# Optimization experiments

Measured on AMD Instinct MI355X. Metric: run time of the kernel, lower is better.

Reference implementation:

```python
import jax, jax.numpy as jnp
import numpy as np

B, S, D, H = 2, 2048, 1024, 16
HD = D // H

def setup_inputs() -> dict:
    key = jax.random.key(0)
    ks = jax.random.split(key, 5)
    s = 1.0 / np.sqrt(D)
    return {
        "x": jax.random.normal(ks[0], (B, S, D), dtype=jnp.float32),
        "Wq": jax.random.normal(ks[1], (D, D), dtype=jnp.float32) * s,
        "Wk": jax.random.normal(ks[2], (D, D), dtype=jnp.float32) * s,
        "Wv": jax.random.normal(ks[3], (D, D), dtype=jnp.float32) * s,
        "Wo": jax.random.normal(ks[4], (D, D), dtype=jnp.float32) * s,
        "bo": jnp.zeros((D,), dtype=jnp.float32),
    }

def reference(x, Wq, Wk, Wv, Wo, bo):
    b, n, _ = x.shape
    # QKV projections (no bias), reshape to [B, H, S, HD]
    def proj(W):
        return (x @ W.T).reshape(b, n, H, HD).transpose(0, 2, 1, 3)
    q, k, v = proj(Wq), proj(Wk), proj(Wv)
    scores = jnp.einsum("bhqd,bhkd->bhqk", q, k)
    causal = jnp.triu(jnp.ones((n, n), dtype=bool), k=1)
    scores = jnp.where(causal, -jnp.inf, scores)
    attn = jax.nn.softmax(scores / np.sqrt(HD), axis=-1)  # dropout p=0.0 (eval)
    ctx = jnp.einsum("bhqk,bhkd->bhqd", attn, v)
    ctx = ctx.transpose(0, 2, 1, 3).reshape(b, n, D)
    return ctx @ Wo.T + bo
```

## Files before the change

### kernel.cpp

```cpp
#include <hip/hip_runtime.h>
#include <stdint.h>


typedef __bf16 bf16_t;
typedef __bf16 bf16x8 __attribute__((ext_vector_type(8)));
typedef float  f32x4  __attribute__((ext_vector_type(4)));
typedef uint32_t u32x4 __attribute__((ext_vector_type(4)));

#define MFMA16(A, B, C) __builtin_amdgcn_mfma_f32_16x16x32_bf16(A, B, C, 0, 0, 0)

__device__ __forceinline__ void async_ld16(const bf16_t* g, bf16_t* l) {
  __builtin_amdgcn_global_load_lds(
      (const __attribute__((address_space(1))) void*)g,
      (__attribute__((address_space(3))) void*)l, 16, 0, 0);
}

__global__ __launch_bounds__(256) void cvt_x(const float* __restrict__ s,
                                             bf16_t* __restrict__ d) {
  const int i4 = (blockIdx.x * 256 + threadIdx.x) * 4;
  const float4 v = *(const float4*)(s + i4);
  union { uint64_t u; bf16_t h[4]; } pk;
  pk.h[0] = (bf16_t)v.x; pk.h[1] = (bf16_t)v.y;
  pk.h[2] = (bf16_t)v.z; pk.h[3] = (bf16_t)v.w;
  *(uint64_t*)(d + i4) = pk.u;
}

__global__ __launch_bounds__(256) void cvt_w3(
    const float* __restrict__ s0, const float* __restrict__ s1,
    const float* __restrict__ s2, bf16_t* __restrict__ d0,
    bf16_t* __restrict__ d1, bf16_t* __restrict__ d2) {
  const int z = blockIdx.y;
  const float* s = (z == 0) ? s0 : (z == 1) ? s1 : s2;
  bf16_t*      d = (z == 0) ? d0 : (z == 1) ? d1 : d2;
  const int i4 = (blockIdx.x * 256 + threadIdx.x) * 4;
  const float4 v = *(const float4*)(s + i4);
  union { uint64_t u; bf16_t h[4]; } pk;
  pk.h[0] = (bf16_t)v.x; pk.h[1] = (bf16_t)v.y;
  pk.h[2] = (bf16_t)v.z; pk.h[3] = (bf16_t)v.w;
  *(uint64_t*)(d + i4) = pk.u;
}

__device__ __forceinline__ void gemm_core_async(const bf16_t* __restrict__ A,
                                                const bf16_t* __restrict__ W,
                                                bf16_t* __restrict__ D,
                                                float* __restrict__ Dout,
                                                const float* __restrict__ bias,
                                                int mode) {
  __shared__ __align__(16) bf16_t As[128 * 64];
  __shared__ __align__(16) bf16_t Bs[128 * 64];

  const int tid  = threadIdx.x;
  const int lane = tid & 63;
  const int w    = tid >> 6;
  const int quad = lane >> 4;
  const int l15  = lane & 15;
  const int bm   = blockIdx.y * 128;
  const int bn   = blockIdx.x * 128;
  const int wm   = (w >> 1) * 64;
  const int wn   = (w & 1) * 64;
  const int sr   = lane >> 3;
  const int sc   = lane & 7;

  f32x4 acc[4][4] = {};

  for (int k0 = 0; k0 < 1024; k0 += 64) {
#pragma unroll
    for (int j = 0; j < 4; ++j) {
      const int r0 = w * 32 + j * 8;
      const int r  = r0 + sr;
      const int c  = sc ^ (r & 7);
      async_ld16(A + (size_t)(bm + r) * 1024 + k0 + c * 8, &As[r0 * 64]);
      async_ld16(W + (size_t)(bn + r) * 1024 + k0 + c * 8, &Bs[r0 * 64]);
    }
    __syncthreads();
#pragma unroll
    for (int kk = 0; kk < 64; kk += 32) {
      const int ck = (kk >> 3) + quad;
      bf16x8 aF[4], bF[4];
#pragma unroll
      for (int mt = 0; mt < 4; ++mt) {
        const int r = wm + mt * 16 + l15;
        aF[mt] = *(const bf16x8*)&As[r * 64 + (ck ^ (r & 7)) * 8];
      }
#pragma unroll
      for (int nt = 0; nt < 4; ++nt) {
        const int r = wn + nt * 16 + l15;
        bF[nt] = *(const bf16x8*)&Bs[r * 64 + (ck ^ (r & 7)) * 8];
      }
#pragma unroll
      for (int mt = 0; mt < 4; ++mt)
#pragma unroll
        for (int nt = 0; nt < 4; ++nt)
          acc[mt][nt] = MFMA16(aF[mt], bF[nt], acc[mt][nt]);
    }
    __syncthreads();
  }

#pragma unroll
  for (int mt = 0; mt < 4; ++mt) {
#pragma unroll
    for (int nt = 0; nt < 4; ++nt) {
      const int n  = bn + wn + nt * 16 + l15;
      const int mb = bm + wm + mt * 16 + quad * 4;
      if (mode == 0) {
        const int h = n >> 6, hd = n & 63;
#pragma unroll
        for (int r = 0; r < 4; ++r) {
          const int m = mb + r;
          const int b = m >> 11, s = m & 2047;
          D[(size_t)b * 2097152 + (size_t)h * 131072 + (size_t)s * 64 + hd] =
              (bf16_t)acc[mt][nt][r];
        }
      } else if (mode == 1) {
        const int h = n >> 6, hd = n & 63;
        const int b = mb >> 11, s0 = mb & 2047;
        union { uint64_t u; bf16_t h4[4]; } pk;
#pragma unroll
        for (int r = 0; r < 4; ++r) pk.h4[r] = (bf16_t)acc[mt][nt][r];
        *(uint64_t*)(D + (size_t)b * 2097152 + (size_t)h * 131072 +
                     (size_t)hd * 2048 + s0) = pk.u;
      } else {
        const float bv = bias[n];
#pragma unroll
        for (int r = 0; r < 4; ++r) {
          const int m = mb + r;
          Dout[(size_t)m * 1024 + n] = acc[mt][nt][r] + bv;
        }
      }
    }
  }
}

__global__ __launch_bounds__(256, 2) void gemm_qkv_a(
    const bf16_t* __restrict__ X,  const bf16_t* __restrict__ Wq,
    const bf16_t* __restrict__ Wk, const bf16_t* __restrict__ Wv,
    bf16_t* __restrict__ Q, bf16_t* __restrict__ K, bf16_t* __restrict__ V) {
  const int z = blockIdx.z;
  const bf16_t* W = (z == 0) ? Wq : (z == 1) ? Wk : Wv;
  bf16_t*       D = (z == 0) ? Q  : (z == 1) ? K  : V;
  gemm_core_async(X, W, D, nullptr, nullptr, (z == 2) ? 1 : 0);
}

__global__ __launch_bounds__(256, 2) void gemm_out_a(
    const bf16_t* __restrict__ ctx, const bf16_t* __restrict__ Wo,
    float* __restrict__ out, const float* __restrict__ bo) {
  gemm_core_async(ctx, Wo, nullptr, out, bo, 2);
}

__global__ __launch_bounds__(256, 2) void attn(
    const bf16_t* __restrict__ Qw, const bf16_t* __restrict__ Kw,
    const bf16_t* __restrict__ Vw, bf16_t* __restrict__ ctx) {
  constexpr int LDK = 72, LDV = 136, LDP = 136;
  __shared__ __align__(16) bf16_t Ks[128 * LDK];
  __shared__ __align__(16) bf16_t Vts[64 * LDV];
  __shared__ __align__(16) bf16_t Ps[128 * LDP];

  const int tid  = threadIdx.x;
  const int lane = tid & 63;
  const int w    = tid >> 6;
  const int quad = lane >> 4;
  const int l15  = lane & 15;
  const int b    = blockIdx.z;
  const int qt   = (b == 0) ? blockIdx.x : 15 - blockIdx.x;
  const int h    = blockIdx.y;
  const size_t bh = (size_t)(b * 16 + h) * (size_t)(2048 * 64);
  const bf16_t* Qh = Qw + bh;
  const bf16_t* Kh = Kw + bh;
  const bf16_t* Vh = Vw + bh;

  const int srow = tid >> 3, schk = tid & 7;
  const int vrow = tid >> 4, vchk = tid & 15;

  bf16_t* Qs = Ps;
  {
    u32x4 rq[4];
#pragma unroll
    for (int s2 = 0; s2 < 4; ++s2)
      rq[s2] = *(const u32x4*)(Qh + (size_t)(qt * 128 + srow + s2 * 32) * 64 + schk * 8);
#pragma unroll
    for (int s2 = 0; s2 < 4; ++s2)
      *(u32x4*)&Qs[(srow + s2 * 32) * LDK + schk * 8] = rq[s2];
  }
  __syncthreads();
  bf16x8 qF[2][2];
#pragma unroll
  for (int kq = 0; kq < 2; ++kq)
#pragma unroll
    for (int k2 = 0; k2 < 2; ++k2)
      qF[kq][k2] = *(const bf16x8*)
          &Qs[(w * 32 + kq * 16 + l15) * LDK + k2 * 32 + quad * 8];

  f32x4 O[2][4] = {};
  float mrow[2] = {-1e30f, -1e30f};
  float lrow[2] = {0.f, 0.f};

  const float sc_log2 = 0.125f * 1.44269504088896340736f;

  u32x4 rk[4], rv[4];
#pragma unroll
  for (int s2 = 0; s2 < 4; ++s2)
    rk[s2] = *(const u32x4*)(Kh + (size_t)(srow + s2 * 32) * 64 + schk * 8);
#pragma unroll
  for (int s2 = 0; s2 < 4; ++s2)
    rv[s2] = *(const u32x4*)(Vh + (size_t)(vrow + s2 * 16) * 2048 + vchk * 8);

  for (int kt = 0; kt <= qt; ++kt) {
    __syncthreads();
#pragma unroll
    for (int s2 = 0; s2 < 4; ++s2)
      *(u32x4*)&Ks[(srow + s2 * 32) * LDK + schk * 8] = rk[s2];
#pragma unroll
    for (int s2 = 0; s2 < 4; ++s2)
      *(u32x4*)&Vts[(vrow + s2 * 16) * LDV + vchk * 8] = rv[s2];
    __syncthreads();

    if (kt < qt) {
      const int kn = kt + 1;
#pragma unroll
      for (int s2 = 0; s2 < 4; ++s2)
        rk[s2] = *(const u32x4*)(Kh + (size_t)(kn * 128 + srow + s2 * 32) * 64 + schk * 8);
#pragma unroll
      for (int s2 = 0; s2 < 4; ++s2)
        rv[s2] = *(const u32x4*)(Vh + (size_t)(vrow + s2 * 16) * 2048 + kn * 128 + vchk * 8);
    }

    f32x4 St[2][8] = {};
#pragma unroll
    for (int ntk = 0; ntk < 8; ++ntk) {
      const int kr = ntk * 16 + l15;
#pragma unroll
      for (int k2 = 0; k2 < 2; ++k2) {
        const bf16x8 kF = *(const bf16x8*)&Ks[kr * LDK + k2 * 32 + quad * 8];
#pragma unroll
        for (int kq = 0; kq < 2; ++kq)
          St[kq][ntk] = MFMA16(kF, qF[kq][k2], St[kq][ntk]);
      }
    }

    if (kt == qt) {
#pragma unroll
      for (int kq = 0; kq < 2; ++kq) {
        const int ql = w * 32 + kq * 16 + l15;
#pragma unroll
        for (int ntk = 0; ntk < 8; ++ntk)
#pragma unroll
          for (int r = 0; r < 4; ++r)
            if (ntk * 16 + quad * 4 + r > ql) St[kq][ntk][r] = -1e30f;
      }
    }

    float aq[2];
#pragma unroll
    for (int kq = 0; kq < 2; ++kq) {
      float mx = -1e30f;
#pragma unroll
      for (int ntk = 0; ntk < 8; ++ntk)
#pragma unroll
        for (int r = 0; r < 4; ++r) mx = fmaxf(mx, St[kq][ntk][r]);
      mx = fmaxf(mx, __shfl_xor(mx, 16));
      mx = fmaxf(mx, __shfl_xor(mx, 32));
      const float mnew  = fmaxf(mrow[kq], mx);
      const float alpha = exp2f((mrow[kq] - mnew) * sc_log2);
      mrow[kq] = mnew;
      float rs = 0.f;
#pragma unroll
      for (int ntk = 0; ntk < 8; ++ntk) {
        union { uint64_t u; bf16_t h4[4]; } pk;
#pragma unroll
        for (int r = 0; r < 4; ++r) {
          const float p = exp2f((St[kq][ntk][r] - mnew) * sc_log2);
          rs += p;
          pk.h4[r] = (bf16_t)p;
        }
        *(uint64_t*)&Ps[(w * 32 + kq * 16 + l15) * LDP + ntk * 16 + quad * 4] = pk.u;
      }
      rs += __shfl_xor(rs, 16);
      rs += __shfl_xor(rs, 32);
      lrow[kq] = lrow[kq] * alpha + rs;
      aq[kq] = alpha;
    }

#pragma unroll
    for (int mt = 0; mt < 2; ++mt) {
#pragma unroll
      for (int r = 0; r < 4; ++r) {
        const float a = __shfl(aq[mt], quad * 4 + r);
#pragma unroll
        for (int nt = 0; nt < 4; ++nt) O[mt][nt][r] *= a;
      }
    }

#pragma unroll
    for (int kk = 0; kk < 128; kk += 32) {
      const int co = kk + quad * 8;
      bf16x8 pF[2], vF[4];
#pragma unroll
      for (int mt = 0; mt < 2; ++mt)
        pF[mt] = *(const bf16x8*)&Ps[(w * 32 + mt * 16 + l15) * LDP + co];
#pragma unroll
      for (int nt = 0; nt < 4; ++nt)
        vF[nt] = *(const bf16x8*)&Vts[(nt * 16 + l15) * LDV + co];
#pragma unroll
      for (int mt = 0; mt < 2; ++mt)
#pragma unroll
        for (int nt = 0; nt < 4; ++nt)
          O[mt][nt] = MFMA16(pF[mt], vF[nt], O[mt][nt]);
    }
  }

#pragma unroll
  for (int mt = 0; mt < 2; ++mt) {
#pragma unroll
    for (int r = 0; r < 4; ++r) {
      const float lr = __shfl(lrow[mt], quad * 4 + r);
      const float iv = 1.f / lr;
      const int s = qt * 128 + w * 32 + mt * 16 + quad * 4 + r;
#pragma unroll
      for (int nt = 0; nt < 4; ++nt) {
        const int hd = nt * 16 + l15;
        ctx[(size_t)(b * 2048 + s) * 1024 + h * 64 + hd] =
            (bf16_t)(O[mt][nt][r] * iv);
      }
    }
  }
}

extern "C" void kernel_launch(void* const* d_in, const int* in_sizes, int n_in,
                              void* d_out, int out_size, void* d_ws, size_t ws_size,
                              hipStream_t stream) {
  const float* x  = (const float*)d_in[0];
  const float* Wq = (const float*)d_in[1];
  const float* Wk = (const float*)d_in[2];
  const float* Wv = (const float*)d_in[3];
  const float* Wo = (const float*)d_in[4];
  const float* bo = (const float*)d_in[5];

  bf16_t* ws   = (bf16_t*)d_ws;
  bf16_t* Qw   = ws;
  bf16_t* Kw   = ws + 4194304;
  bf16_t* Vw   = ws + 8388608;
  bf16_t* ctxw = ws + 12582912;
  bf16_t* Wob  = Qw;

  bf16_t* dscr = (bf16_t*)d_out;
  bf16_t* xb   = dscr;
  bf16_t* Wqb  = dscr + 4194304;
  bf16_t* Wkb  = dscr + 5242880;
  bf16_t* Wvb  = dscr + 6291456;
  float*  out  = (float*)d_out;

  dim3 blk(256);
  cvt_x<<<dim3(4096), blk, 0, stream>>>(x, xb);
  cvt_w3<<<dim3(1024, 3), blk, 0, stream>>>(Wq, Wk, Wv, Wqb, Wkb, Wvb);
  gemm_qkv_a<<<dim3(8, 32, 3), blk, 0, stream>>>(xb, Wqb, Wkb, Wvb, Qw, Kw, Vw);
  attn<<<dim3(16, 16, 2), blk, 0, stream>>>(Qw, Kw, Vw, ctxw);
  cvt_x<<<dim3(1024), blk, 0, stream>>>(Wo, Wob);
  gemm_out_a<<<dim3(8, 32, 1), blk, 0, stream>>>(ctxw, Wob, out, bo);
}
```

Before: 190.8 us.

## Pair causal query tiles per attention block and merge conversion kernels

Each attention block now handles two query tiles, qt and 15-qt, one after the other. Every block therefore does the same causal work, and the grid shrinks to 256 blocks, which removes tail imbalance from uneven causal rows. The x and QKV weight conversions are also merged into one launch to save launch overhead. The cost is fewer, longer blocks, which may lower occupancy across the GPU's many CUs, plus a grid where 3/4 of the blocks in the merged conversion exit at once.

```diff
diff --git a/kernel.cpp b/kernel.cpp
--- a/kernel.cpp
+++ b/kernel.cpp
@@ -15,9 +15,7 @@
       (__attribute__((address_space(3))) void*)l, 16, 0, 0);
 }
 
-__global__ __launch_bounds__(256) void cvt_x(const float* __restrict__ s,
-                                             bf16_t* __restrict__ d) {
-  const int i4 = (blockIdx.x * 256 + threadIdx.x) * 4;
+__device__ __forceinline__ void cvt4(const float* s, bf16_t* d, int i4) {
   const float4 v = *(const float4*)(s + i4);
   union { uint64_t u; bf16_t h[4]; } pk;
   pk.h[0] = (bf16_t)v.x; pk.h[1] = (bf16_t)v.y;
@@ -25,19 +23,22 @@
   *(uint64_t*)(d + i4) = pk.u;
 }
 
-__global__ __launch_bounds__(256) void cvt_w3(
-    const float* __restrict__ s0, const float* __restrict__ s1,
-    const float* __restrict__ s2, bf16_t* __restrict__ d0,
-    bf16_t* __restrict__ d1, bf16_t* __restrict__ d2) {
-  const int z = blockIdx.y;
-  const float* s = (z == 0) ? s0 : (z == 1) ? s1 : s2;
-  bf16_t*      d = (z == 0) ? d0 : (z == 1) ? d1 : d2;
+__global__ __launch_bounds__(256) void cvt_all(
+    const float* __restrict__ sx, const float* __restrict__ s1,
+    const float* __restrict__ s2, const float* __restrict__ s3,
+    bf16_t* __restrict__ dx, bf16_t* __restrict__ d1,
+    bf16_t* __restrict__ d2, bf16_t* __restrict__ d3) {
+  const int y = blockIdx.y;
+  if (y != 0 && blockIdx.x >= 1024) return;
   const int i4 = (blockIdx.x * 256 + threadIdx.x) * 4;
-  const float4 v = *(const float4*)(s + i4);
-  union { uint64_t u; bf16_t h[4]; } pk;
-  pk.h[0] = (bf16_t)v.x; pk.h[1] = (bf16_t)v.y;
-  pk.h[2] = (bf16_t)v.z; pk.h[3] = (bf16_t)v.w;
-  *(uint64_t*)(d + i4) = pk.u;
+  const float* s = (y == 0) ? sx : (y == 1) ? s1 : (y == 2) ? s2 : s3;
+  bf16_t*      d = (y == 0) ? dx : (y == 1) ? d1 : (y == 2) ? d2 : d3;
+  cvt4(s, d, i4);
+}
+
+__global__ __launch_bounds__(256) void cvt_one(const float* __restrict__ s,
+                                               bf16_t* __restrict__ d) {
+  cvt4(s, d, (blockIdx.x * 256 + threadIdx.x) * 4);
 }
 
 __device__ __forceinline__ void gemm_core_async(const bf16_t* __restrict__ A,
@@ -161,7 +162,6 @@
   const int quad = lane >> 4;
   const int l15  = lane & 15;
   const int b    = blockIdx.z;
-  const int qt   = (b == 0) ? blockIdx.x : 15 - blockIdx.x;
   const int h    = blockIdx.y;
   const size_t bh = (size_t)(b * 16 + h) * (size_t)(2048 * 64);
   const bf16_t* Qh = Qw + bh;
@@ -171,155 +171,160 @@
   const int srow = tid >> 3, schk = tid & 7;
   const int vrow = tid >> 4, vchk = tid & 15;
 
-  bf16_t* Qs = Ps;
-  {
-    u32x4 rq[4];
+  const float sc_log2 = 0.125f * 1.44269504088896340736f;
+
+  for (int pass = 0; pass < 2; ++pass) {
+    const int qt = (pass == 0) ? blockIdx.x : 15 - blockIdx.x;
+
+    __syncthreads();
+    bf16_t* Qs = Ps;
+    {
+      u32x4 rq[4];
+#pragma unroll
+      for (int s2 = 0; s2 < 4; ++s2)
+        rq[s2] = *(const u32x4*)(Qh + (size_t)(qt * 128 + srow + s2 * 32) * 64 + schk * 8);
+#pragma unroll
+      for (int s2 = 0; s2 < 4; ++s2)
+        *(u32x4*)&Qs[(srow + s2 * 32) * LDK + schk * 8] = rq[s2];
+    }
+    __syncthreads();
+    bf16x8 qF[2][2];
+#pragma unroll
+    for (int kq = 0; kq < 2; ++kq)
+#pragma unroll
+      for (int k2 = 0; k2 < 2; ++k2)
+        qF[kq][k2] = *(const bf16x8*)
+            &Qs[(w * 32 + kq * 16 + l15) * LDK + k2 * 32 + quad * 8];
+
+    f32x4 O[2][4] = {};
+    float mrow[2] = {-1e30f, -1e30f};
+    float lrow[2] = {0.f, 0.f};
+
+    u32x4 rk[4], rv[4];
 #pragma unroll
     for (int s2 = 0; s2 < 4; ++s2)
-      rq[s2] = *(const u32x4*)(Qh + (size_t)(qt * 128 + srow + s2 * 32) * 64 + schk * 8);
+      rk[s2] = *(const u32x4*)(Kh + (size_t)(srow + s2 * 32) * 64 + schk * 8);
 #pragma unroll
     for (int s2 = 0; s2 < 4; ++s2)
-      *(u32x4*)&Qs[(srow + s2 * 32) * LDK + schk * 8] = rq[s2];
-  }
-  __syncthreads();
-  bf16x8 qF[2][2];
-#pragma unroll
-  for (int kq = 0; kq < 2; ++kq)
-#pragma unroll
-    for (int k2 = 0; k2 < 2; ++k2)
-      qF[kq][k2] = *(const bf16x8*)
-          &Qs[(w * 32 + kq * 16 + l15) * LDK + k2 * 32 + quad * 8];
-
-  f32x4 O[2][4] = {};
-  float mrow[2] = {-1e30f, -1e30f};
-  float lrow[2] = {0.f, 0.f};
-
-  const float sc_log2 = 0.125f * 1.44269504088896340736f;
-
-  u32x4 rk[4], rv[4];
-#pragma unroll
-  for (int s2 = 0; s2 < 4; ++s2)
-    rk[s2] = *(const u32x4*)(Kh + (size_t)(srow + s2 * 32) * 64 + schk * 8);
-#pragma unroll
-  for (int s2 = 0; s2 < 4; ++s2)
-    rv[s2] = *(const u32x4*)(Vh + (size_t)(vrow + s2 * 16) * 2048 + vchk * 8);
-
-  for (int kt = 0; kt <= qt; ++kt) {
-    __syncthreads();
-#pragma unroll
-    for (int s2 = 0; s2 < 4; ++s2)
-      *(u32x4*)&Ks[(srow + s2 * 32) * LDK + schk * 8] = rk[s2];
-#pragma unroll
-    for (int s2 = 0; s2 < 4; ++s2)
-      *(u32x4*)&Vts[(vrow + s2 * 16) * LDV + vchk * 8] = rv[s2];
-    __syncthreads();
-
-    if (kt < qt) {
-      const int kn = kt + 1;
+      rv[s2] = *(const u32x4*)(Vh + (size_t)(vrow + s2 * 16) * 2048 + vchk * 8);
+
+    for (int kt = 0; kt <= qt; ++kt) {
+      __syncthreads();
 #pragma unroll
       for (int s2 = 0; s2 < 4; ++s2)
-        rk[s2] = *(const u32x4*)(Kh + (size_t)(kn * 128 + srow + s2 * 32) * 64 + schk * 8);
+        *(u32x4*)&Ks[(srow + s2 * 32) * LDK + schk * 8] = rk[s2];
 #pragma unroll
       for (int s2 = 0; s2 < 4; ++s2)
-        rv[s2] = *(const u32x4*)(Vh + (size_t)(vrow + s2 * 16) * 2048 + kn * 128 + vchk * 8);
-    }
-
-    f32x4 St[2][8] = {};
-#pragma unroll
-    for (int ntk = 0; ntk < 8; ++ntk) {
-      const int kr = ntk * 16 + l15;
-#pragma unroll
-      for (int k2 = 0; k2 < 2; ++k2) {
-        const bf16x8 kF = *(const bf16x8*)&Ks[kr * LDK + k2 * 32 + quad * 8];
-#pragma unroll
-        for (int kq = 0; kq < 2; ++kq)
-          St[kq][ntk] = MFMA16(kF, qF[kq][k2], St[kq][ntk]);
-      }
-    }
-
-    if (kt == qt) {
+        *(u32x4*)&Vts[(vrow + s2 * 16) * LDV + vchk * 8] = rv[s2];
+      __syncthreads();
+
+      if (kt < qt) {
+        const int kn = kt + 1;
+#pragma unroll
+        for (int s2 = 0; s2 < 4; ++s2)
+          rk[s2] = *(const u32x4*)(Kh + (size_t)(kn * 128 + srow + s2 * 32) * 64 + schk * 8);
+#pragma unroll
+        for (int s2 = 0; s2 < 4; ++s2)
+          rv[s2] = *(const u32x4*)(Vh + (size_t)(vrow + s2 * 16) * 2048 + kn * 128 + vchk * 8);
+      }
+
+      f32x4 St[2][8] = {};
+#pragma unroll
+      for (int ntk = 0; ntk < 8; ++ntk) {
+        const int kr = ntk * 16 + l15;
+#pragma unroll
+        for (int k2 = 0; k2 < 2; ++k2) {
+          const bf16x8 kF = *(const bf16x8*)&Ks[kr * LDK + k2 * 32 + quad * 8];
+#pragma unroll
+          for (int kq = 0; kq < 2; ++kq)
+            St[kq][ntk] = MFMA16(kF, qF[kq][k2], St[kq][ntk]);
+        }
+      }
+
+      if (kt == qt) {
+#pragma unroll
+        for (int kq = 0; kq < 2; ++kq) {
+          const int ql = w * 32 + kq * 16 + l15;
+#pragma unroll
+          for (int ntk = 0; ntk < 8; ++ntk)
+#pragma unroll
+            for (int r = 0; r < 4; ++r)
+              if (ntk * 16 + quad * 4 + r > ql) St[kq][ntk][r] = -1e30f;
+        }
+      }
+
+      float aq[2];
 #pragma unroll
       for (int kq = 0; kq < 2; ++kq) {
-        const int ql = w * 32 + kq * 16 + l15;
+        float mx = -1e30f;
 #pragma unroll
         for (int ntk = 0; ntk < 8; ++ntk)
 #pragma unroll
-          for (int r = 0; r < 4; ++r)
-            if (ntk * 16 + quad * 4 + r > ql) St[kq][ntk][r] = -1e30f;
-      }
-    }
-
-    float aq[2];
-#pragma unroll
-    for (int kq = 0; kq < 2; ++kq) {
-      float mx = -1e30f;
-#pragma unroll
-      for (int ntk = 0; ntk < 8; ++ntk)
-#pragma unroll
-        for (int r = 0; r < 4; ++r) mx = fmaxf(mx, St[kq][ntk][r]);
-      mx = fmaxf(mx, __shfl_xor(mx, 16));
-      mx = fmaxf(mx, __shfl_xor(mx, 32));
-      const float mnew  = fmaxf(mrow[kq], mx);
-      const float alpha = exp2f((mrow[kq] - mnew) * sc_log2);
-      mrow[kq] = mnew;
-      float rs = 0.f;
-#pragma unroll
-      for (int ntk = 0; ntk < 8; ++ntk) {
-        union { uint64_t u; bf16_t h4[4]; } pk;
+          for (int r = 0; r < 4; ++r) mx = fmaxf(mx, St[kq][ntk][r]);
+        mx = fmaxf(mx, __shfl_xor(mx, 16));
+        mx = fmaxf(mx, __shfl_xor(mx, 32));
+        const float mnew  = fmaxf(mrow[kq], mx);
+        const float alpha = exp2f((mrow[kq] - mnew) * sc_log2);
+        mrow[kq] = mnew;
+        float rs = 0.f;
+#pragma unroll
+        for (int ntk = 0; ntk < 8; ++ntk) {
+          union { uint64_t u; bf16_t h4[4]; } pk;
+#pragma unroll
+          for (int r = 0; r < 4; ++r) {
+            const float p = exp2f((St[kq][ntk][r] - mnew) * sc_log2);
+            rs += p;
+            pk.h4[r] = (bf16_t)p;
+          }
+          *(uint64_t*)&Ps[(w * 32 + kq * 16 + l15) * LDP + ntk * 16 + quad * 4] = pk.u;
+        }
+        rs += __shfl_xor(rs, 16);
+        rs += __shfl_xor(rs, 32);
+        lrow[kq] = lrow[kq] * alpha + rs;
+        aq[kq] = alpha;
+      }
+
+#pragma unroll
+      for (int mt = 0; mt < 2; ++mt) {
 #pragma unroll
         for (int r = 0; r < 4; ++r) {
-          const float p = exp2f((St[kq][ntk][r] - mnew) * sc_log2);
-          rs += p;
-          pk.h4[r] = (bf16_t)p;
-        }
-        *(uint64_t*)&Ps[(w * 32 + kq * 16 + l15) * LDP + ntk * 16 + quad * 4] = pk.u;
-      }
-      rs += __shfl_xor(rs, 16);
-      rs += __shfl_xor(rs, 32);
-      lrow[kq] = lrow[kq] * alpha + rs;
-      aq[kq] = alpha;
+          const float a = __shfl(aq[mt], quad * 4 + r);
+#pragma unroll
+          for (int nt = 0; nt < 4; ++nt) O[mt][nt][r] *= a;
+        }
+      }
+
+#pragma unroll
+      for (int kk = 0; kk < 128; kk += 32) {
+        const int co = kk + quad * 8;
+        bf16x8 pF[2], vF[4];
+#pragma unroll
+        for (int mt = 0; mt < 2; ++mt)
+          pF[mt] = *(const bf16x8*)&Ps[(w * 32 + mt * 16 + l15) * LDP + co];
+#pragma unroll
+        for (int nt = 0; nt < 4; ++nt)
+          vF[nt] = *(const bf16x8*)&Vts[(nt * 16 + l15) * LDV + co];
+#pragma unroll
+        for (int mt = 0; mt < 2; ++mt)
+#pragma unroll
+          for (int nt = 0; nt < 4; ++nt)
+            O[mt][nt] = MFMA16(pF[mt], vF[nt], O[mt][nt]);
+      }
     }
 
 #pragma unroll
     for (int mt = 0; mt < 2; ++mt) {
 #pragma unroll
       for (int r = 0; r < 4; ++r) {
-        const float a = __shfl(aq[mt], quad * 4 + r);
-#pragma unroll
-        for (int nt = 0; nt < 4; ++nt) O[mt][nt][r] *= a;
-      }
-    }
-
-#pragma unroll
-    for (int kk = 0; kk < 128; kk += 32) {
-      const int co = kk + quad * 8;
-      bf16x8 pF[2], vF[4];
-#pragma unroll
-      for (int mt = 0; mt < 2; ++mt)
-        pF[mt] = *(const bf16x8*)&Ps[(w * 32 + mt * 16 + l15) * LDP + co];
-#pragma unroll
-      for (int nt = 0; nt < 4; ++nt)
-        vF[nt] = *(const bf16x8*)&Vts[(nt * 16 + l15) * LDV + co];
-#pragma unroll
-      for (int mt = 0; mt < 2; ++mt)
-#pragma unroll
-        for (int nt = 0; nt < 4; ++nt)
-          O[mt][nt] = MFMA16(pF[mt], vF[nt], O[mt][nt]);
-    }
-  }
-
-#pragma unroll
-  for (int mt = 0; mt < 2; ++mt) {
-#pragma unroll
-    for (int r = 0; r < 4; ++r) {
-      const float lr = __shfl(lrow[mt], quad * 4 + r);
-      const float iv = 1.f / lr;
-      const int s = qt * 128 + w * 32 + mt * 16 + quad * 4 + r;
-#pragma unroll
-      for (int nt = 0; nt < 4; ++nt) {
-        const int hd = nt * 16 + l15;
-        ctx[(size_t)(b * 2048 + s) * 1024 + h * 64 + hd] =
-            (bf16_t)(O[mt][nt][r] * iv);
+        const float lr = __shfl(lrow[mt], quad * 4 + r);
+        const float iv = 1.f / lr;
+        const int s = qt * 128 + w * 32 + mt * 16 + quad * 4 + r;
+#pragma unroll
+        for (int nt = 0; nt < 4; ++nt) {
+          const int hd = nt * 16 + l15;
+          ctx[(size_t)(b * 2048 + s) * 1024 + h * 64 + hd] =
+              (bf16_t)(O[mt][nt][r] * iv);
+        }
       }
     }
   }
@@ -350,10 +355,9 @@
   float*  out  = (float*)d_out;
 
   dim3 blk(256);
-  cvt_x<<<dim3(4096), blk, 0, stream>>>(x, xb);
-  cvt_w3<<<dim3(1024, 3), blk, 0, stream>>>(Wq, Wk, Wv, Wqb, Wkb, Wvb);
+  cvt_all<<<dim3(4096, 4), blk, 0, stream>>>(x, Wq, Wk, Wv, xb, Wqb, Wkb, Wvb);
   gemm_qkv_a<<<dim3(8, 32, 3), blk, 0, stream>>>(xb, Wqb, Wkb, Wvb, Qw, Kw, Vw);
-  attn<<<dim3(16, 16, 2), blk, 0, stream>>>(Qw, Kw, Vw, ctxw);
-  cvt_x<<<dim3(1024), blk, 0, stream>>>(Wo, Wob);
+  attn<<<dim3(8, 16, 2), blk, 0, stream>>>(Qw, Kw, Vw, ctxw);
+  cvt_one<<<dim3(1024), blk, 0, stream>>>(Wo, Wob);
   gemm_out_a<<<dim3(8, 32, 1), blk, 0, stream>>>(ctxw, Wob, out, bo);
 }
```

After: 194.8 us. 2.1% more time.
